# Kernel optimization log

Measured on AMD Instinct MI355X. Metric: run time of the kernel, lower is better.

The kernel has to match this reference:

```python
import jax, jax.numpy as jnp
import numpy as np

B, T, D = 4, 8192, 1024
H = 16
HD = D // H  # 64
TOP_K = 64


def setup_inputs() -> dict:
    key = jax.random.key(0)
    ks = jax.random.split(key, 6)
    x = jax.random.normal(ks[0], (B, T, D), dtype=jnp.float32)
    # torch nn.Linear weights are [out, in]; y = x @ W.T
    Wq = jax.random.normal(ks[1], (D, D), dtype=jnp.float32) * 0.02
    Wk = jax.random.normal(ks[2], (D, D), dtype=jnp.float32) * 0.02
    Wv = jax.random.normal(ks[3], (D, D), dtype=jnp.float32) * 0.02
    Wo = jax.random.normal(ks[4], (D, D), dtype=jnp.float32) * 0.02
    # indexer: nn.Linear(head_dim, 1, bias=False) -> weight [1, HD]; keep as [HD]
    w_score = jax.random.normal(ks[5], (HD,), dtype=jnp.float32) * 0.02
    return {"x": x, "Wq": Wq, "Wk": Wk, "Wv": Wv, "Wo": Wo, "w_score": w_score}


def reference(x, Wq, Wk, Wv, Wo, w_score):
    b, t, d = x.shape
    top_k = min(TOP_K, t)
    # projections: [B,T,D] -> [B,H,T,HD]
    def proj(W):
        return jnp.einsum('btd,ed->bte', x, W).reshape(b, t, H, HD).transpose(0, 2, 1, 3)
    q = proj(Wq)
    k = proj(Wk)
    v = proj(Wv)
    # lightning indexer scores: [B,H,T]
    idx_scores = jnp.einsum('bhtd,d->bht', k, w_score)
    _, top_idx = jax.lax.top_k(idx_scores, top_k)  # [B,H,K]
    idx = top_idx[..., None]  # [B,H,K,1]
    k_sparse = jnp.take_along_axis(k, idx, axis=2)  # [B,H,K,HD]
    v_sparse = jnp.take_along_axis(v, idx, axis=2)
    scale = HD ** -0.5
    scores = jnp.einsum('bhtd,bhkd->bhtk', q, k_sparse) * scale  # [B,H,T,K]
    attn = jax.nn.softmax(scores, axis=-1)
    out = jnp.einsum('bhtk,bhkd->bhtd', attn, v_sparse)  # [B,H,T,HD]
    out = out.transpose(0, 2, 1, 3).reshape(b, t, d)
    return jnp.einsum('btd,ed->bte', out, Wo)
```

## Files before the change

### kernel.cpp

```cpp
#include <hip/hip_runtime.h>
#include <hip/hip_bf16.h>
#include <stdint.h>

#define NB 4
#define NT 8192
#define ND 1024
#define NH 16
#define NHD 64
#define NK 64
#define NM (NB*NT)

typedef __attribute__((ext_vector_type(4))) float f32x4;
typedef __attribute__((ext_vector_type(8))) short s16x8;
typedef const void __attribute__((address_space(1)))* gas1_t;
typedef void __attribute__((address_space(3)))* las3_t;

__device__ __forceinline__ float bf2f(ushort u) {
  union { uint32_t i; float f; } v; v.i = ((uint32_t)u) << 16; return v.f;
}
__device__ __forceinline__ ushort f2bf(float f) {
  union { float f; uint32_t i; } v; v.f = f;
  uint32_t r = v.i + 0x7FFFu + ((v.i >> 16) & 1u);
  return (ushort)(r >> 16);
}
__device__ __forceinline__ uint32_t f2ord(uint32_t u) {
  return (u & 0x80000000u) ? ~u : (u | 0x80000000u);
}

__global__ __launch_bounds__(256) void convert_w_kernel(
    const float* __restrict__ Wq, const float* __restrict__ Wk,
    const float* __restrict__ Wv, const float* __restrict__ Wo,
    ushort* __restrict__ wqb, ushort* __restrict__ wkb,
    ushort* __restrict__ wvb, ushort* __restrict__ wob) {
  int i = blockIdx.x * 256 + threadIdx.x;
  wqb[i] = f2bf(Wq[i]); wkb[i] = f2bf(Wk[i]);
  wvb[i] = f2bf(Wv[i]); wob[i] = f2bf(Wo[i]);
}

__global__ __launch_bounds__(256) void prep_u_kernel(
    const float* __restrict__ Wk, const float* __restrict__ wscore,
    float* __restrict__ u) {
  int e = (blockIdx.x & 3) * 256 + threadIdx.x;
  int h = blockIdx.x >> 2;
  float acc = 0.f;
  #pragma unroll 8
  for (int d = 0; d < NHD; ++d) acc += wscore[d] * Wk[(size_t)(h*NHD + d)*ND + e];
  u[h*ND + e] = acc;
}

__global__ __launch_bounds__(256) void prep_x_kernel(
    const float* __restrict__ x, const float* __restrict__ u,
    ushort* __restrict__ xb, float* __restrict__ scores) {
  __shared__ float pbuf[16][4][5];
  int t = threadIdx.x, w = t >> 6, l = t & 63;
  int e0 = w * 256 + l * 4;
  int bid = blockIdx.x;
  int c = bid & 7, q = (bid >> 3) & 3, a = bid >> 5;
  int j = a * 8 + c;
  int q4 = q * 4;
  f32x4 uv[4];
  #pragma unroll
  for (int h = 0; h < 4; ++h) uv[h] = *(const f32x4*)(u + (q4 + h) * ND + e0);
  #pragma unroll
  for (int h = 0; h < 4; ++h) asm volatile("" : "+v"(uv[h]));
  int row0 = j * 32;
  int boff = ((row0 >> 13) << 4);
  int tt0 = row0 & (NT - 1);
  for (int batch = 0; batch < 2; ++batch) {
    #pragma unroll 2
    for (int rr = 0; rr < 16; ++rr) {
      int row = row0 + batch * 16 + rr;
      f32x4 xv = *(const f32x4*)(x + (size_t)row * ND + e0);
      if (q == 0) {
        ushort4 o; o.x = f2bf(xv[0]); o.y = f2bf(xv[1]); o.z = f2bf(xv[2]); o.w = f2bf(xv[3]);
        *(ushort4*)(xb + (size_t)row * ND + e0) = o;
      }
      float p[4];
      #pragma unroll
      for (int h = 0; h < 4; ++h)
        p[h] = xv[0]*uv[h][0] + xv[1]*uv[h][1] + xv[2]*uv[h][2] + xv[3]*uv[h][3];
      float q2[2];
      #pragma unroll
      for (int jj = 0; jj < 2; ++jj) {
        bool hi = (l & 1);
        float keep = hi ? p[2*jj+1] : p[2*jj];
        float send = hi ? p[2*jj]   : p[2*jj+1];
        q2[jj] = keep + __shfl_xor(send, 1, 64);
      }
      float q1;
      {
        bool hi = ((l >> 1) & 1);
        float keep = hi ? q2[1] : q2[0];
        float send = hi ? q2[0] : q2[1];
        q1 = keep + __shfl_xor(send, 2, 64);
      }
      q1 += __shfl_xor(q1, 4, 64);
      q1 += __shfl_xor(q1, 8, 64);
      q1 += __shfl_xor(q1, 16, 64);
      q1 += __shfl_xor(q1, 32, 64);
      if (l < 4) pbuf[rr][w][l] = q1;
    }
    __syncthreads();
    if (t < 64) {
      int r16 = t & 15, h = t >> 4;
      float s = pbuf[r16][0][h] + pbuf[r16][1][h] + pbuf[r16][2][h] + pbuf[r16][3][h];
      scores[(size_t)(boff + q4 + h) * NT + tt0 + batch * 16 + r16] = s;
    }
    __syncthreads();
  }
}

__global__ __launch_bounds__(256) void topk_kernel(
    const float* __restrict__ scores, int* __restrict__ tidx) {
  int bh = blockIdx.x, t = threadIdx.x;
  __shared__ uint32_t keys[NT];
  __shared__ int hist[4096];
  __shared__ uint32_t ck[512];
  __shared__ int ci[512];
  __shared__ int chunksum[256];
  __shared__ int s_binB, s_c0;
  __shared__ int cnt_hi, cnt_cand;

  for (int i = t; i < 4096; i += 256) hist[i] = 0;
  if (t == 0) { cnt_hi = 0; cnt_cand = 0; }
  __syncthreads();
  const uint4* sg = (const uint4*)(scores + (size_t)bh * NT);
  for (int i = t; i < NT/4; i += 256) {
    uint4 v = sg[i];
    uint32_t k0 = f2ord(v.x), k1 = f2ord(v.y), k2 = f2ord(v.z), k3 = f2ord(v.w);
    keys[i*4+0] = k0; keys[i*4+1] = k1; keys[i*4+2] = k2; keys[i*4+3] = k3;
    atomicAdd(&hist[k0 >> 20], 1); atomicAdd(&hist[k1 >> 20], 1);
    atomicAdd(&hist[k2 >> 20], 1); atomicAdd(&hist[k3 >> 20], 1);
  }
  __syncthreads();
  {
    int hi = 4095 - t * 16;
    int s = 0;
    #pragma unroll
    for (int j = 0; j < 16; ++j) s += hist[hi - j];
    chunksum[t] = s;
  }
  __syncthreads();
  if (t == 0) {
    int cum = 0, c = 0;
    while (cum + chunksum[c] < NK) { cum += chunksum[c]; ++c; }
    int bin = 4095 - c * 16;
    while (cum + hist[bin] < NK) { cum += hist[bin]; --bin; }
    s_binB = bin; s_c0 = cum;
  }
  __syncthreads();
  int binB = s_binB, c0 = s_c0;
  for (int i = t; i < NT; i += 256) {
    int b = keys[i] >> 20;
    if (b > binB) {
      int p = atomicAdd(&cnt_hi, 1);
      tidx[bh*NK + p] = i;
    } else if (b == binB) {
      int p = atomicAdd(&cnt_cand, 1);
      if (p < 512) { ck[p] = keys[i]; ci[p] = i; }
    }
  }
  __syncthreads();
  int nc = cnt_cand; if (nc > 512) nc = 512;
  int need = NK - c0;
  for (int p = t; p < nc; p += 256) {
    uint32_t myk = ck[p]; int myi = ci[p];
    int rank = 0;
    for (int j = 0; j < nc; ++j) {
      uint32_t kj = ck[j];
      rank += (kj > myk || (kj == myk && ci[j] < myi)) ? 1 : 0;
    }
    if (rank < need) tidx[bh*NK + c0 + rank] = myi;
  }
}

__global__ __launch_bounds__(256, 4) void sparse_kv_kernel(
    const ushort* __restrict__ xb, const ushort* __restrict__ wkb,
    const ushort* __restrict__ wvb, const int* __restrict__ tidx,
    ushort* __restrict__ ksp, ushort* __restrict__ vtsp) {
  int bh = blockIdx.x, gy = blockIdx.y;
  int b = bh >> 4, h = bh & 15;
  int t = threadIdx.x;
  __shared__ __align__(16) ushort xl[16][128];
  __shared__ int kid[16];
  if (t < 16) kid[t] = tidx[bh*NK + gy*16 + t];
  int d = t & 63, kq = t >> 6;
  float ak[4] = {0.f,0.f,0.f,0.f}, av[4] = {0.f,0.f,0.f,0.f};
  const ushort* wkr = wkb + (size_t)(h*NHD + d) * ND;
  const ushort* wvr = wvb + (size_t)(h*NHD + d) * ND;
  for (int kc = 0; kc < ND; kc += 128) {
    __syncthreads();
    {
      int row = t >> 4, c8 = (t & 15) * 8;
      *(uint4*)&xl[row][c8] = *(const uint4*)(xb + (size_t)(b*NT + kid[row]) * ND + kc + c8);
    }
    __syncthreads();
    #pragma unroll 1
    for (int sub = 0; sub < 8; ++sub) {
      s16x8 k0 = *(const s16x8*)(wkr + kc + sub*16);
      s16x8 k1 = *(const s16x8*)(wkr + kc + sub*16 + 8);
      s16x8 v0 = *(const s16x8*)(wvr + kc + sub*16);
      s16x8 v1 = *(const s16x8*)(wvr + kc + sub*16 + 8);
      float kf[16], vf2[16];
      #pragma unroll
      for (int j = 0; j < 8; ++j) {
        kf[j]  = bf2f((ushort)k0[j]); kf[8+j]  = bf2f((ushort)k1[j]);
        vf2[j] = bf2f((ushort)v0[j]); vf2[8+j] = bf2f((ushort)v1[j]);
      }
      #pragma unroll
      for (int kk = 0; kk < 4; ++kk) {
        #pragma unroll
        for (int j = 0; j < 16; ++j) {
          float xvv = bf2f(xl[kq*4 + kk][sub*16 + j]);
          ak[kk] += xvv * kf[j];
          av[kk] += xvv * vf2[j];
        }
      }
    }
  }
  #pragma unroll
  for (int kk = 0; kk < 4; ++kk) {
    int key = gy*16 + kq*4 + kk;
    ksp[((size_t)bh*NK + key)*NHD + d] = f2bf(ak[kk]);
    vtsp[((size_t)bh*NHD + d)*NK + key] = f2bf(av[kk]);
  }
}

template<int STORE_BF16>
__global__ __launch_bounds__(512, 2) void gemm8_kernel(
    const ushort* __restrict__ A, const ushort* __restrict__ Bw,
    void* __restrict__ Cout) {
  __shared__ __align__(16) char lds[131072];
  const int t = threadIdx.x, wid = t >> 6, l = t & 63;
  const int wr = wid >> 2, wc = wid & 3;
  int bid = blockIdx.x;
  int wg = (bid & 7) * 64 + (bid >> 3);
  int tm = wg >> 2, tn = wg & 3;
  const int K = 1024, N = 1024;
  const ushort* Ab = A + (size_t)tm * 256 * K;
  const ushort* Bb = Bw + (size_t)tn * 256 * K;
  const int skh  = ((l & 3) * 8) ^ (((l >> 5) & 1) << 4);
  const int srow = l >> 2;
  const int lane_off = (l & 15) * 64 + ((((l >> 4) * 8) ^ (((l >> 3) & 1) << 4)) * 2);
  f32x4 acc[8][4];
  #pragma unroll
  for (int i = 0; i < 8; ++i)
    #pragma unroll
    for (int j = 0; j < 4; ++j) acc[i][j] = (f32x4){0.f, 0.f, 0.f, 0.f};
  s16x8 afr[4][2], bfr[2][2];

#define STG(gbase, matoff, half, ktile, buf) do { \
    const ushort* _s = (gbase) + (size_t)((half)*128 + wid*16 + srow) * K + (ktile)*64 + skh; \
    int _d = (buf)*65536 + (matoff) + ((half)*128 + wid*16)*64; \
    __builtin_amdgcn_global_load_lds((gas1_t)_s, (las3_t)(lds + _d), 16, 0, 0); \
    __builtin_amdgcn_global_load_lds((gas1_t)(_s + 32), (las3_t)(lds + _d + 16384), 16, 0, 0); \
  } while (0)

#define RD_A(mh, kh, buf) do { \
    _Pragma("unroll") \
    for (int mi = 0; mi < 4; ++mi) \
      afr[mi][kh] = *(const s16x8*)(lds + (buf)*65536 + (kh)*16384 + \
                      ((((mh)*2 + wr)*64 + mi*16))*64 + lane_off); \
  } while (0)

#define RD_B(nh, kh, buf) do { \
    _Pragma("unroll") \
    for (int ni = 0; ni < 2; ++ni) \
      bfr[ni][kh] = *(const s16x8*)(lds + (buf)*65536 + 32768 + (kh)*16384 + \
                      (((nh)*128 + wc*32 + ni*16))*64 + lane_off); \
  } while (0)

#define MMAQH(mh, nh, kh) do { \
    __builtin_amdgcn_s_setprio(1); \
    _Pragma("unroll") \
    for (int mi = 0; mi < 4; ++mi) \
      _Pragma("unroll") \
      for (int ni = 0; ni < 2; ++ni) \
        acc[(mh)*4+mi][(nh)*2+ni] = __builtin_amdgcn_mfma_f32_16x16x32_bf16( \
            afr[mi][kh], bfr[ni][kh], acc[(mh)*4+mi][(nh)*2+ni], 0, 0, 0); \
    __builtin_amdgcn_s_setprio(0); \
  } while (0)

#define LG0() do { asm volatile("s_waitcnt lgkmcnt(0)" ::: "memory"); \
                   __builtin_amdgcn_sched_barrier(0); } while (0)
#define ENDPH() do { __builtin_amdgcn_sched_barrier(0); \
                     __builtin_amdgcn_s_barrier(); } while (0)

#define TILE(kt, bc, bn) do { \
  LG0(); MMAQH(0,0,0); RD_A(0,1,bc); RD_B(0,1,bc); ENDPH(); \
  LG0(); MMAQH(0,0,1); RD_B(1,0,bc); \
  if ((kt)+1 < 16) STG(Bb,32768,0,(kt)+1,bn); ENDPH(); \
  LG0(); MMAQH(0,1,0); RD_B(1,1,bc); ENDPH(); \
  LG0(); MMAQH(0,1,1); RD_A(1,0,bc); \
  if ((kt)+2 < 16) STG(Ab,0,0,(kt)+2,bc); ENDPH(); \
  LG0(); MMAQH(1,1,0); RD_A(1,1,bc); ENDPH(); \
  LG0(); MMAQH(1,1,1); RD_B(0,0,bc); \
  if ((kt)+2 < 16) STG(Bb,32768,1,(kt)+2,bc); ENDPH(); \
  LG0(); MMAQH(1,0,0); RD_B(0,1,bc); ENDPH(); \
  LG0(); MMAQH(1,0,1); \
  if ((kt) < 14)       { asm volatile("s_waitcnt vmcnt(4)" ::: "memory"); } \
  else if ((kt) == 14) { asm volatile("s_waitcnt vmcnt(0)" ::: "memory"); } \
  __builtin_amdgcn_sched_barrier(0); \
  __builtin_amdgcn_s_barrier(); \
  if ((kt)+1 < 16) { RD_A(0,0,bn); RD_B(0,0,bn); } \
  if ((kt)+2 < 16) STG(Ab,0,1,(kt)+2,bc); \
} while (0)

  STG(Ab,0,0,0,0); STG(Bb,32768,0,0,0); STG(Ab,0,1,0,0); STG(Bb,32768,1,0,0);
  STG(Ab,0,0,1,1); STG(Bb,32768,1,1,1); STG(Ab,0,1,1,1);
  asm volatile("s_waitcnt vmcnt(6)" ::: "memory");
  __builtin_amdgcn_s_barrier();
  RD_A(0,0,0); RD_B(0,0,0);

  for (int k2 = 0; k2 < 8; ++k2) {
    TILE(2*k2,     0, 1);
    TILE(2*k2 + 1, 1, 0);
  }
#undef TILE
#undef STG
#undef RD_A
#undef RD_B
#undef MMAQH
#undef LG0
#undef ENDPH

  #pragma unroll
  for (int mi8 = 0; mi8 < 8; ++mi8) {
    int grow = tm*256 + (((mi8 >> 2)*2 + wr)*64) + (mi8 & 3)*16 + (l >> 4)*4;
    #pragma unroll
    for (int ni4 = 0; ni4 < 4; ++ni4) {
      int gcol = tn*256 + (ni4 >> 1)*128 + wc*32 + (ni4 & 1)*16 + (l & 15);
      #pragma unroll
      for (int r = 0; r < 4; ++r) {
        size_t off = (size_t)(grow + r) * N + gcol;
        if (STORE_BF16) ((ushort*)Cout)[off] = f2bf(acc[mi8][ni4][r]);
        else            ((float*)Cout)[off]  = acc[mi8][ni4][r];
      }
    }
  }
}

__global__ __launch_bounds__(256, 2) void attn_kernel(
    const ushort* __restrict__ qg, const ushort* __restrict__ ksp,
    const ushort* __restrict__ vtsp, ushort* __restrict__ aout) {
  int bh = blockIdx.y;
  int b = bh >> 4, h = bh & 15;
  int t = threadIdx.x, w = t >> 6, l = t & 63;
  __shared__ __align__(16) ushort Pl[4][1024];
  const ushort* kb = ksp + (size_t)bh * NK * NHD;
  const ushort* vb = vtsp + (size_t)bh * NHD * NK;
  s16x8 kf[2][4], vf[2][4];
  #pragma unroll
  for (int ks = 0; ks < 2; ++ks)
    #pragma unroll
    for (int ni = 0; ni < 4; ++ni) {
      kf[ks][ni] = *(const s16x8*)&kb[(size_t)(ni*16 + (l & 15))*NHD + ks*32 + (l >> 4)*8];
      vf[ks][ni] = *(const s16x8*)&vb[(size_t)(ni*16 + (l & 15))*NK + ks*32 + (l >> 4)*8];
    }
  int rowbase = blockIdx.x * 256 + w * 64;
  #pragma unroll 1
  for (int mi = 0; mi < 4; ++mi) {
    int r0 = rowbase + mi * 16;
    s16x8 af[2];
    #pragma unroll
    for (int ks = 0; ks < 2; ++ks)
      af[ks] = *(const s16x8*)&qg[(size_t)(b*NT + r0 + (l & 15))*ND + h*NHD + ks*32 + (l >> 4)*8];
    f32x4 sc[4];
    #pragma unroll
    for (int ni = 0; ni < 4; ++ni) {
      f32x4 z; z[0]=0.f; z[1]=0.f; z[2]=0.f; z[3]=0.f;
      z = __builtin_amdgcn_mfma_f32_16x16x32_bf16(af[0], kf[0][ni], z, 0, 0, 0);
      sc[ni] = __builtin_amdgcn_mfma_f32_16x16x32_bf16(af[1], kf[1][ni], z, 0, 0, 0);
    }
    #pragma unroll
    for (int r = 0; r < 4; ++r) {
      float v0 = sc[0][r]*0.125f, v1 = sc[1][r]*0.125f;
      float v2 = sc[2][r]*0.125f, v3 = sc[3][r]*0.125f;
      float m = fmaxf(fmaxf(v0, v1), fmaxf(v2, v3));
      #pragma unroll
      for (int mm = 8; mm >= 1; mm >>= 1) m = fmaxf(m, __shfl_xor(m, mm, 64));
      float e0 = __expf(v0 - m), e1 = __expf(v1 - m);
      float e2 = __expf(v2 - m), e3 = __expf(v3 - m);
      float s = e0 + e1 + e2 + e3;
      #pragma unroll
      for (int mm = 8; mm >= 1; mm >>= 1) s += __shfl_xor(s, mm, 64);
      float inv = 1.f / s;
      int prow = (l >> 4)*4 + r;
      int lo = l & 7, hb = (l >> 3) & 1, sw = prow & 7;
      Pl[w][prow*64 + ((0 + hb) ^ sw)*8 + lo] = f2bf(e0 * inv);
      Pl[w][prow*64 + ((2 + hb) ^ sw)*8 + lo] = f2bf(e1 * inv);
      Pl[w][prow*64 + ((4 + hb) ^ sw)*8 + lo] = f2bf(e2 * inv);
      Pl[w][prow*64 + ((6 + hb) ^ sw)*8 + lo] = f2bf(e3 * inv);
    }
    s16x8 pf[2];
    #pragma unroll
    for (int ks = 0; ks < 2; ++ks)
      pf[ks] = *(const s16x8*)&Pl[w][(l & 15)*64 + ((ks*4 + (l >> 4)) ^ (l & 7))*8];
    f32x4 oc[4];
    #pragma unroll
    for (int ni = 0; ni < 4; ++ni) {
      f32x4 z; z[0]=0.f; z[1]=0.f; z[2]=0.f; z[3]=0.f;
      z = __builtin_amdgcn_mfma_f32_16x16x32_bf16(pf[0], vf[0][ni], z, 0, 0, 0);
      oc[ni] = __builtin_amdgcn_mfma_f32_16x16x32_bf16(pf[1], vf[1][ni], z, 0, 0, 0);
    }
    #pragma unroll
    for (int ni = 0; ni < 4; ++ni)
      #pragma unroll
      for (int r = 0; r < 4; ++r) {
        int row = r0 + (l >> 4)*4 + r;
        aout[(size_t)(b*NT + row)*ND + h*NHD + ni*16 + (l & 15)] = f2bf(oc[ni][r]);
      }
  }
}

extern "C" void kernel_launch(void* const* d_in, const int* in_sizes, int n_in,
                              void* d_out, int out_size, void* d_ws, size_t ws_size,
                              hipStream_t stream) {
  (void)in_sizes; (void)n_in; (void)out_size; (void)ws_size;
  const float* x  = (const float*)d_in[0];
  const float* Wq = (const float*)d_in[1];
  const float* Wk = (const float*)d_in[2];
  const float* Wv = (const float*)d_in[3];
  const float* Wo = (const float*)d_in[4];
  const float* wscore = (const float*)d_in[5];

  char* base = (char*)d_ws;
  ushort* xb     = (ushort*)(base + 0);
  ushort* qb     = (ushort*)(base + 67108864);
  float*  scores = (float*) (base + 134217728);
  float*  u      = (float*) (base + 136314880);
  ushort* wqb    = (ushort*)(base + 136380416);
  ushort* wkb    = (ushort*)(base + 138477568);
  ushort* wvb    = (ushort*)(base + 140574720);
  ushort* wob    = (ushort*)(base + 142671872);
  int*    tidx   = (int*)   (base + 144769024);
  ushort* ksp    = (ushort*)(base + 144785408);
  ushort* vtsp   = (ushort*)(base + 145309696);
  ushort* aout   = xb;

  convert_w_kernel<<<dim3(4096), dim3(256), 0, stream>>>(Wq, Wk, Wv, Wo, wqb, wkb, wvb, wob);
  prep_u_kernel<<<dim3(64), dim3(256), 0, stream>>>(Wk, wscore, u);
  prep_x_kernel<<<dim3(4096), dim3(256), 0, stream>>>(x, u, xb, scores);
  topk_kernel<<<dim3(64), dim3(256), 0, stream>>>(scores, tidx);
  sparse_kv_kernel<<<dim3(64, 4), dim3(256), 0, stream>>>(xb, wkb, wvb, tidx, ksp, vtsp);
  gemm8_kernel<1><<<dim3(512), dim3(512), 0, stream>>>(xb, wqb, (void*)qb);
  attn_kernel<<<dim3(32, 64), dim3(256), 0, stream>>>(qb, ksp, vtsp, aout);
  gemm8_kernel<0><<<dim3(512), dim3(512), 0, stream>>>(aout, wob, d_out);
}
```

Before: 318.3 us.

## Compute indexer scores for all heads with split-bf16 MFMA, reading x once

Rewrites prep_x so each block covers 32 tokens and all 16 heads, using bf16 MFMA with hi/lo splits of x and u (three MFMAs) to keep near-fp32 precision. Previously each row of x was re-read by four blocks, one per group of four heads, using scalar FMAs and shuffle reductions. The new form cuts x traffic and moves the dot products onto matrix units, at the cost of extra conversion work and a small precision change from the split-bf16 approximation.

```diff
diff --git a/kernel.cpp b/kernel.cpp
--- a/kernel.cpp
+++ b/kernel.cpp
@@ -39,74 +39,67 @@
 
 __global__ __launch_bounds__(256) void prep_u_kernel(
     const float* __restrict__ Wk, const float* __restrict__ wscore,
-    float* __restrict__ u) {
+    ushort* __restrict__ uhi, ushort* __restrict__ ulo) {
   int e = (blockIdx.x & 3) * 256 + threadIdx.x;
   int h = blockIdx.x >> 2;
   float acc = 0.f;
   #pragma unroll 8
   for (int d = 0; d < NHD; ++d) acc += wscore[d] * Wk[(size_t)(h*NHD + d)*ND + e];
-  u[h*ND + e] = acc;
+  ushort hv = f2bf(acc);
+  uhi[h*ND + e] = hv;
+  ulo[h*ND + e] = f2bf(acc - bf2f(hv));
 }
 
 __global__ __launch_bounds__(256) void prep_x_kernel(
-    const float* __restrict__ x, const float* __restrict__ u,
-    ushort* __restrict__ xb, float* __restrict__ scores) {
-  __shared__ float pbuf[16][4][5];
+    const float* __restrict__ x, const ushort* __restrict__ uhi,
+    const ushort* __restrict__ ulo, ushort* __restrict__ xb,
+    float* __restrict__ scores) {
+  __shared__ float red[4][2][16][17];
   int t = threadIdx.x, w = t >> 6, l = t & 63;
-  int e0 = w * 256 + l * 4;
-  int bid = blockIdx.x;
-  int c = bid & 7, q = (bid >> 3) & 3, a = bid >> 5;
-  int j = a * 8 + c;
-  int q4 = q * 4;
-  f32x4 uv[4];
-  #pragma unroll
-  for (int h = 0; h < 4; ++h) uv[h] = *(const f32x4*)(u + (q4 + h) * ND + e0);
-  #pragma unroll
-  for (int h = 0; h < 4; ++h) asm volatile("" : "+v"(uv[h]));
-  int row0 = j * 32;
-  int boff = ((row0 >> 13) << 4);
-  int tt0 = row0 & (NT - 1);
-  for (int batch = 0; batch < 2; ++batch) {
-    #pragma unroll 2
-    for (int rr = 0; rr < 16; ++rr) {
-      int row = row0 + batch * 16 + rr;
-      f32x4 xv = *(const f32x4*)(x + (size_t)row * ND + e0);
-      if (q == 0) {
-        ushort4 o; o.x = f2bf(xv[0]); o.y = f2bf(xv[1]); o.z = f2bf(xv[2]); o.w = f2bf(xv[3]);
-        *(ushort4*)(xb + (size_t)row * ND + e0) = o;
+  int tok0 = blockIdx.x * 32;
+  int rs = l & 15, ks8 = (l >> 4) * 8;
+  f32x4 acc[2];
+  acc[0] = (f32x4){0.f,0.f,0.f,0.f};
+  acc[1] = (f32x4){0.f,0.f,0.f,0.f};
+  #pragma unroll 2
+  for (int ks = 0; ks < 8; ++ks) {
+    int kb = w * 256 + ks * 32;
+    s16x8 bh = *(const s16x8*)(uhi + rs * ND + kb + ks8);
+    s16x8 bl = *(const s16x8*)(ulo + rs * ND + kb + ks8);
+    #pragma unroll
+    for (int mi = 0; mi < 2; ++mi) {
+      const float* xr = x + (size_t)(tok0 + mi*16 + rs) * ND + kb + ks8;
+      f32x4 x0 = *(const f32x4*)xr;
+      f32x4 x1 = *(const f32x4*)(xr + 4);
+      s16x8 hi, lo;
+      #pragma unroll
+      for (int j = 0; j < 4; ++j) {
+        ushort h0 = f2bf(x0[j]);
+        hi[j] = (short)h0; lo[j] = (short)f2bf(x0[j] - bf2f(h0));
+        ushort h1 = f2bf(x1[j]);
+        hi[4+j] = (short)h1; lo[4+j] = (short)f2bf(x1[j] - bf2f(h1));
       }
-      float p[4];
-      #pragma unroll
-      for (int h = 0; h < 4; ++h)
-        p[h] = xv[0]*uv[h][0] + xv[1]*uv[h][1] + xv[2]*uv[h][2] + xv[3]*uv[h][3];
-      float q2[2];
-      #pragma unroll
-      for (int jj = 0; jj < 2; ++jj) {
-        bool hi = (l & 1);
-        float keep = hi ? p[2*jj+1] : p[2*jj];
-        float send = hi ? p[2*jj]   : p[2*jj+1];
-        q2[jj] = keep + __shfl_xor(send, 1, 64);
-      }
-      float q1;
-      {
-        bool hi = ((l >> 1) & 1);
-        float keep = hi ? q2[1] : q2[0];
-        float send = hi ? q2[0] : q2[1];
-        q1 = keep + __shfl_xor(send, 2, 64);
-      }
-      q1 += __shfl_xor(q1, 4, 64);
-      q1 += __shfl_xor(q1, 8, 64);
-      q1 += __shfl_xor(q1, 16, 64);
-      q1 += __shfl_xor(q1, 32, 64);
-      if (l < 4) pbuf[rr][w][l] = q1;
-    }
-    __syncthreads();
-    if (t < 64) {
-      int r16 = t & 15, h = t >> 4;
-      float s = pbuf[r16][0][h] + pbuf[r16][1][h] + pbuf[r16][2][h] + pbuf[r16][3][h];
-      scores[(size_t)(boff + q4 + h) * NT + tt0 + batch * 16 + r16] = s;
-    }
-    __syncthreads();
+      *(s16x8*)(xb + (size_t)(tok0 + mi*16 + rs) * ND + kb + ks8) = hi;
+      acc[mi] = __builtin_amdgcn_mfma_f32_16x16x32_bf16(hi, bh, acc[mi], 0, 0, 0);
+      acc[mi] = __builtin_amdgcn_mfma_f32_16x16x32_bf16(lo, bh, acc[mi], 0, 0, 0);
+      acc[mi] = __builtin_amdgcn_mfma_f32_16x16x32_bf16(hi, bl, acc[mi], 0, 0, 0);
+    }
+  }
+  #pragma unroll
+  for (int mi = 0; mi < 2; ++mi)
+    #pragma unroll
+    for (int r = 0; r < 4; ++r)
+      red[w][mi][(l >> 4) * 4 + r][l & 15] = acc[mi][r];
+  __syncthreads();
+  int boff = ((tok0 >> 13) << 4);
+  int tt0 = tok0 & (NT - 1);
+  #pragma unroll
+  for (int it = 0; it < 2; ++it) {
+    int tok = t & 31, h = (t >> 5) + it * 8;
+    int mi = tok >> 4, row = tok & 15;
+    float s = red[0][mi][row][h] + red[1][mi][row][h]
+            + red[2][mi][row][h] + red[3][mi][row][h];
+    scores[(size_t)(boff + h) * NT + tt0 + tok] = s;
   }
 }
 
@@ -428,7 +421,8 @@
   ushort* xb     = (ushort*)(base + 0);
   ushort* qb     = (ushort*)(base + 67108864);
   float*  scores = (float*) (base + 134217728);
-  float*  u      = (float*) (base + 136314880);
+  ushort* uhi    = (ushort*)(base + 136314880);
+  ushort* ulo    = (ushort*)(base + 136347648);
   ushort* wqb    = (ushort*)(base + 136380416);
   ushort* wkb    = (ushort*)(base + 138477568);
   ushort* wvb    = (ushort*)(base + 140574720);
@@ -439,8 +433,8 @@
   ushort* aout   = xb;
 
   convert_w_kernel<<<dim3(4096), dim3(256), 0, stream>>>(Wq, Wk, Wv, Wo, wqb, wkb, wvb, wob);
-  prep_u_kernel<<<dim3(64), dim3(256), 0, stream>>>(Wk, wscore, u);
-  prep_x_kernel<<<dim3(4096), dim3(256), 0, stream>>>(x, u, xb, scores);
+  prep_u_kernel<<<dim3(64), dim3(256), 0, stream>>>(Wk, wscore, uhi, ulo);
+  prep_x_kernel<<<dim3(1024), dim3(256), 0, stream>>>(x, uhi, ulo, xb, scores);
   topk_kernel<<<dim3(64), dim3(256), 0, stream>>>(scores, tidx);
   sparse_kv_kernel<<<dim3(64, 4), dim3(256), 0, stream>>>(xb, wkb, wvb, tidx, ksp, vtsp);
   gemm8_kernel<1><<<dim3(512), dim3(512), 0, stream>>>(xb, wqb, (void*)qb);
```

Result: faster. 295.7 us (-7.1%).
